# Kernel tuning notes

Measured on AMD Instinct MI355X. Metric: run time of the kernel, lower is better.

Reference implementation:

```python
import jax, jax.numpy as jnp
import numpy as np

B, R, C1, C2, C3, K, NC = 512, 200, 32, 32, 512, 8, 2
RATIO = 0.5
K1 = int(np.ceil(RATIO * R))    # 100 nodes kept after pool1
K2 = int(np.ceil(RATIO * K1))   # 50 nodes kept after pool2
EDGE_P = 0.1
NEG = -1e9
BN_EPS = 1e-5
LEAK = 0.01


def setup_inputs() -> dict:
    key = jax.random.key(0)
    ks = jax.random.split(key, 12)

    def lin_w(k, o, i):
        return (jax.random.normal(k, (o, i)) / np.sqrt(i)).astype(jnp.float32)

    return {
        "x": jax.random.normal(ks[0], (B, R, R), dtype=jnp.float32),
        "adj": jax.random.uniform(ks[1], (B, R, R), dtype=jnp.float32),
        "roi": jnp.arange(R, dtype=jnp.int32),
        # conv1 ROI-conditioned weight net: Linear(R->K) -> ReLU -> Linear(K->R*C1)
        "W1a": lin_w(ks[2], K, R), "b1a": jnp.zeros((K,), jnp.float32),
        "W2a": lin_w(ks[3], R * C1, K), "b2a": jnp.zeros((R * C1,), jnp.float32),
        "bias1": jnp.zeros((C1,), jnp.float32),
        # conv2 ROI-conditioned weight net: Linear(R->K) -> ReLU -> Linear(K->C1*C2)
        "W1b": lin_w(ks[4], K, R), "b1b": jnp.zeros((K,), jnp.float32),
        "W2b": lin_w(ks[5], C1 * C2, K), "b2b": jnp.zeros((C1 * C2,), jnp.float32),
        "bias2": jnp.zeros((C2,), jnp.float32),
        # TopK pooling projection vectors
        "wp1": jax.random.normal(ks[6], (C1,), dtype=jnp.float32),
        "wp2": jax.random.normal(ks[7], (C2,), dtype=jnp.float32),
        # MLP head
        "Wm1": lin_w(ks[8], C2, (C1 + C2) * 2), "bm1": jnp.zeros((C2,), jnp.float32),
        "g1": jnp.ones((C2,), jnp.float32), "be1": jnp.zeros((C2,), jnp.float32),
        "Wm2": lin_w(ks[9], C3, C2), "bm2": jnp.zeros((C3,), jnp.float32),
        "g2": jnp.ones((C3,), jnp.float32), "be2": jnp.zeros((C3,), jnp.float32),
        "Ws": lin_w(ks[10], NC, C3), "bs": jnp.zeros((NC,), jnp.float32),
    }


def _nn_table(W1, b1, W2, b2, cin, cout):
    # nn applied to one-hot ROI vectors == table lookup; build the full [R, cin, cout] table once.
    t = jax.nn.relu(W1.T + b1) @ W2.T + b2  # [R, cin*cout]
    return t.reshape(R, cin, cout)


def _gconv(x, w_adj, mask, w_node, bias):
    # per-node ROI-conditioned transform, then edge-softmax weighted aggregation
    if w_node.ndim == 3:   # shared table indexed by arange -> [R,cin,cout]
        xt = jnp.einsum('bni,nio->bno', x, w_node)
    else:                   # gathered per graph -> [B,n,cin,cout]
        xt = jnp.einsum('bni,bnio->bno', x, w_node)
    n = x.shape[1]
    eye = jnp.eye(n, dtype=bool)
    # remove self loops, add self loop with weight 1, softmax over incoming edges
    logits = jnp.where(mask & ~eye, w_adj, NEG)
    logits = jnp.where(eye, 1.0, logits)
    att = jax.nn.softmax(logits, axis=-1)  # row i = incoming edges of node i
    return jnp.einsum('bij,bjo->bio', att, xt) + bias


def _topk_pool(h, w_adj, mask, roi, w, k):
    s = jax.nn.sigmoid(h @ w / jnp.linalg.norm(w))  # [B, n]
    vals, perm = jax.lax.top_k(s, k)
    xs = jnp.take_along_axis(h, perm[:, :, None], axis=1) * vals[:, :, None]
    b = jnp.arange(h.shape[0])[:, None, None]
    w_sub = w_adj[b, perm[:, :, None], perm[:, None, :]]
    m_sub = mask[b, perm[:, :, None], perm[:, None, :]]
    roi_sub = roi[perm] if roi.ndim == 1 else jnp.take_along_axis(roi, perm, axis=1)
    return xs, w_sub, m_sub, roi_sub, vals


def _augment(w_adj, mask):
    # add_self_loops(fill=1) -> spspmm(A, A) -> remove_self_loops, in dense-batched form
    n = w_adj.shape[1]
    eye = jnp.eye(n, dtype=bool)
    wd = jnp.where(mask & ~eye, w_adj, 0.0)
    wd = jnp.where(eye, 1.0, wd)
    a2 = jnp.einsum('bij,bjk->bik', wd, wd)
    m2 = (a2 != 0.0) & ~eye
    a2 = jnp.where(eye, 0.0, a2)
    return a2, m2


def _mlp_block(y, Wl, bl, g, be):
    y = y @ Wl.T + bl
    y = jnp.where(y > 0, y, LEAK * y)          # LeakyReLU(0.01)
    mu = jnp.mean(y, axis=0)
    var = jnp.var(y, axis=0)                    # training-mode BatchNorm1d
    return g * (y - mu) * jax.lax.rsqrt(var + BN_EPS) + be


def _forward(x, adj, roi, W1a, b1a, W2a, b2a, bias1, W1b, b1b, W2b, b2b, bias2,
             wp1, wp2, Wm1, bm1, g1, be1, Wm2, bm2, g2, be2, Ws, bs):
    mask0 = adj < EDGE_P
    wtab1 = _nn_table(W1a, b1a, W2a, b2a, R, C1)   # [R, R, C1]
    h1 = _gconv(x, adj, mask0, wtab1[roi], bias1)  # [B, R, C1]
    x1, w1, m1, roi1, vals1 = _topk_pool(h1, adj, mask0, roi, wp1, K1)
    a_aug, m_aug = _augment(w1, m1)                 # 2-hop augmented adjacency
    wtab2 = _nn_table(W1b, b1b, W2b, b2b, C1, C2)  # [R, C1, C2]
    h2 = _gconv(x1, a_aug, m_aug, wtab2[roi1], bias2)  # [B, K1, C2]
    x2, _, _, _, vals2 = _topk_pool(h2, a_aug, m_aug, roi1, wp2, K2)
    # readout: [gmp, gap] per level, concatenated -> (C1+C2)*2 = 128
    feat = jnp.concatenate([x1.max(1), x1.mean(1), x2.max(1), x2.mean(1)], axis=-1)
    y = _mlp_block(feat, Wm1, bm1, g1, be1)
    y = _mlp_block(y, Wm2, bm2, g2, be2)
    logp = jax.nn.log_softmax(y @ Ws.T + bs, axis=-1)
    return logp, jax.nn.sigmoid(vals1), jax.nn.sigmoid(vals2)


def reference(x, adj, roi, W1a, b1a, W2a, b2a, bias1, W1b, b1b, W2b, b2b, bias2,
              wp1, wp2, Wm1, bm1, g1, be1, Wm2, bm2, g2, be2, Ws, bs):
    logp, s1, s2 = _forward(x, adj, roi, W1a, b1a, W2a, b2a, bias1,
                            W1b, b1b, W2b, b2b, bias2, wp1, wp2,
                            Wm1, bm1, g1, be1, Wm2, bm2, g2, be2, Ws, bs)
    return (logp, wp1, wp2, s1, s2)
```

## Files before the change

kernel.cpp:

```cpp
#include <hip/hip_runtime.h>
#include <math.h>

#define NB 512
#define RR 200
#define KK1 100
#define KK2 50

__device__ __forceinline__ float sigm(float v) { return 1.0f / (1.0f + expf(-v)); }

__global__ void k_tab(const float* __restrict__ W1, const float* __restrict__ b1,
                      const float* __restrict__ W2, const float* __restrict__ b2,
                      float* __restrict__ tab, int OUT) {
  int n = blockIdx.x;
  __shared__ float h[8];
  if (threadIdx.x < 8) {
    float v = W1[threadIdx.x * RR + n] + b1[threadIdx.x];
    h[threadIdx.x] = v > 0.f ? v : 0.f;
  }
  __syncthreads();
  for (int j = threadIdx.x; j < OUT; j += 256) {
    float acc = b2[j];
#pragma unroll
    for (int k = 0; k < 8; k++) acc += h[k] * W2[j * 8 + k];
    tab[(size_t)n * OUT + j] = acc;
  }
}

__global__ void k_norm(const float* __restrict__ wp1, const float* __restrict__ wp2,
                       float* __restrict__ norms) {
  int t = threadIdx.x;
  float a = (t < 32) ? wp1[t] * wp1[t] : 0.f;
  float b = (t < 32) ? wp2[t] * wp2[t] : 0.f;
  for (int s = 32; s; s >>= 1) { a += __shfl_xor(a, s); b += __shfl_xor(b, s); }
  if (t == 0) { norms[0] = sqrtf(a); norms[1] = sqrtf(b); }
}

__global__ __launch_bounds__(1024) void k_xt1(const float* __restrict__ x,
                                              const float* __restrict__ wtab1,
                                              float* __restrict__ xt1) {
  int n = blockIdx.x, t = threadIdx.x;
  __shared__ float wsm[6400];
  for (int idx = t; idx < 1600; idx += 1024)
    *(float4*)&wsm[idx * 4] = *(const float4*)(wtab1 + (size_t)n * 6400 + idx * 4);
  __syncthreads();
  int bg = t >> 3, og = t & 7;
  int b0 = bg * 4;
  const float* xp = x + (size_t)b0 * 40000 + (size_t)n * 200;
  float acc[4][4] = {};
  float4 A[4], Bf[4], N0[4] = {}, N1[4] = {};
#pragma unroll
  for (int r = 0; r < 4; r++) A[r] = *(const float4*)(xp + (size_t)r * 40000);
#pragma unroll
  for (int r = 0; r < 4; r++) Bf[r] = *(const float4*)(xp + (size_t)r * 40000 + 4);
  for (int g = 0; g < 50; g += 2) {
    int i = g * 4;
    if (g + 2 < 50) {
#pragma unroll
      for (int r = 0; r < 4; r++) N0[r] = *(const float4*)(xp + (size_t)r * 40000 + i + 8);
#pragma unroll
      for (int r = 0; r < 4; r++) N1[r] = *(const float4*)(xp + (size_t)r * 40000 + i + 12);
    }
#pragma unroll
    for (int k = 0; k < 4; k++) {
      float4 w4 = *(const float4*)&wsm[(i + k) * 32 + og * 4];
#pragma unroll
      for (int r = 0; r < 4; r++) {
        float xs = (&A[r].x)[k];
        acc[r][0] += xs * w4.x; acc[r][1] += xs * w4.y;
        acc[r][2] += xs * w4.z; acc[r][3] += xs * w4.w;
      }
    }
#pragma unroll
    for (int k = 0; k < 4; k++) {
      float4 w4 = *(const float4*)&wsm[(i + 4 + k) * 32 + og * 4];
#pragma unroll
      for (int r = 0; r < 4; r++) {
        float xs = (&Bf[r].x)[k];
        acc[r][0] += xs * w4.x; acc[r][1] += xs * w4.y;
        acc[r][2] += xs * w4.z; acc[r][3] += xs * w4.w;
      }
    }
#pragma unroll
    for (int r = 0; r < 4; r++) { A[r] = N0[r]; Bf[r] = N1[r]; }
  }
#pragma unroll
  for (int r = 0; r < 4; r++)
    *(float4*)(xt1 + (size_t)(b0 + r) * 6400 + (size_t)n * 32 + og * 4) =
        make_float4(acc[r][0], acc[r][1], acc[r][2], acc[r][3]);
}

__global__ __launch_bounds__(1024) void k_att1(const float* __restrict__ adj,
                                               const float* __restrict__ xt1,
                                               const float* __restrict__ bias1,
                                               const float* __restrict__ wp1,
                                               const float* __restrict__ norms,
                                               float* __restrict__ h1, float* __restrict__ sc1) {
  int t = threadIdx.x;
  __shared__ float2 pvj[16][4][49];
  __shared__ int cntS[16][4];
  int w = t >> 6, lane = t & 63;
  int rq = lane >> 4, cg = lane & 15;
  float2 biasv = *(const float2*)(bias1 + cg * 2);
  float2 wpv = *(const float2*)(wp1 + cg * 2);
  float nrm = norms[0];
  unsigned long long ltmask = (1ull << lane) - 1ull;
  int b = blockIdx.x;
  float av[4][4];
  {
    const float* abase = adj + (size_t)b * 40000 + (size_t)(w * 4) * 200;
#pragma unroll
    for (int r = 0; r < 4; r++)
#pragma unroll
      for (int s2 = 0; s2 < 4; s2++) {
        int j = lane + 64 * s2;
        av[r][s2] = (j < RR) ? __builtin_nontemporal_load(abase + r * 200 + j) : 1.0f;
      }
  }
  for (int rg = w; rg < 50; rg += 16) {
#pragma unroll
    for (int r = 0; r < 4; r++) {
      int i = rg * 4 + r;
      float e[4];
      bool nz[4];
#pragma unroll
      for (int s2 = 0; s2 < 4; s2++) {
        int j = lane + 64 * s2;
        float a = av[r][s2];
        bool keep = (j < RR) && ((j == i) || (a < 0.1f));
        float lg = (j == i) ? 1.0f : a;
        e[s2] = keep ? __expf(lg - 1.0f) : 0.f;
        nz[s2] = keep;
      }
      int base = 0;
#pragma unroll
      for (int s2 = 0; s2 < 4; s2++) {
        unsigned long long m = __ballot(nz[s2]);
        if (nz[s2]) pvj[w][r][base + __popcll(m & ltmask)] = make_float2(e[s2], (float)(lane + 64 * s2));
        base += __popcll(m);
      }
      if (lane == 0) cntS[w][r] = base;
    }
    int rg2 = rg + 16;
    if (rg2 < 50) {
      const float* abase = adj + (size_t)b * 40000 + (size_t)(rg2 * 4) * 200;
#pragma unroll
      for (int r = 0; r < 4; r++)
#pragma unroll
        for (int s2 = 0; s2 < 4; s2++) {
          int j = lane + 64 * s2;
          if (j < RR) av[r][s2] = __builtin_nontemporal_load(abase + r * 200 + j);
        }
    }
    int cnt = cntS[w][rq];
    const float* xtb = xt1 + (size_t)b * 6400 + cg * 2;
    float ax = 0.f, ay = 0.f, lsum = 0.f;
    for (int q = 0; q < cnt; q++) {
      float2 pe = pvj[w][rq][q];
      int jj = (int)pe.y;
      float2 xv = *(const float2*)(xtb + jj * 32);
      lsum += pe.x;
      ax += pe.x * xv.x;
      ay += pe.x * xv.y;
    }
    float inv = 1.0f / lsum;
    int i = rg * 4 + rq;
    float2 hv = make_float2(ax * inv + biasv.x, ay * inv + biasv.y);
    *(float2*)(h1 + ((size_t)b * RR + i) * 32 + cg * 2) = hv;
    float tt = hv.x * wpv.x + hv.y * wpv.y;
    tt += __shfl_xor(tt, 1); tt += __shfl_xor(tt, 2);
    tt += __shfl_xor(tt, 4); tt += __shfl_xor(tt, 8);
    if (cg == 0) sc1[b * RR + i] = sigm(tt / nrm);
  }
}

__global__ void k_top1(const float* __restrict__ sc1, int* __restrict__ perm1,
                       float* __restrict__ vals1, float* __restrict__ out_s1) {
  int b = blockIdx.x, t = threadIdx.x;
  __shared__ float s[RR];
  for (int i = t; i < RR; i += 256) s[i] = sc1[b * RR + i];
  __syncthreads();
  for (int i = t; i < RR; i += 256) {
    float si = s[i];
    int rank = 0;
    for (int j = 0; j < RR; j++) {
      float sj = s[j];
      rank += (sj > si) || (sj == si && j < i);
    }
    if (rank < KK1) {
      perm1[b * KK1 + rank] = i;
      vals1[b * KK1 + rank] = si;
      out_s1[b * KK1 + rank] = sigm(si);
    }
  }
}

__global__ __launch_bounds__(256) void k_stage2a(const float* __restrict__ h1,
                                                 const float* __restrict__ wtab2,
                                                 const int* __restrict__ perm1,
                                                 const float* __restrict__ vals1,
                                                 float* __restrict__ xt2,
                                                 float* __restrict__ feat) {
  int b = blockIdx.x, t = threadIdx.x;
  int kbase = blockIdx.y * 50;
  __shared__ float x1s[KK1 * 33];
  __shared__ int pk[KK1];
  __shared__ float vk[KK1];
  if (t < KK1) { pk[t] = perm1[b * KK1 + t]; vk[t] = vals1[b * KK1 + t]; }
  __syncthreads();
  for (int i = t; i < KK1 * 32; i += 256) {
    int k = i >> 5, o = i & 31;
    x1s[k * 33 + o] = h1[((size_t)b * RR + pk[k]) * 32 + o] * vk[k];
  }
  __syncthreads();
  if (blockIdx.y == 0 && t < 32) {
    float mx = -3e38f, sm = 0.f;
    for (int k = 0; k < KK1; k++) { float v = x1s[k * 33 + t]; mx = fmaxf(mx, v); sm += v; }
    feat[b * 128 + t] = mx;
    feat[b * 128 + 32 + t] = sm / 100.0f;
  }
  int w = t >> 6, lane = t & 63;
  int og = lane & 7, kq = lane >> 3;
#pragma unroll
  for (int pass = 0; pass < 2; pass++) {
    int kl = pass * 32 + w * 8 + kq;
    if (kl < 50) {
      int kg = kbase + kl;
      const float* W = wtab2 + (size_t)pk[kg] * 1024 + og * 4;
      float4 a4 = make_float4(0.f, 0.f, 0.f, 0.f);
#pragma unroll 8
      for (int ii = 0; ii < 32; ii++) {
        float4 w4 = *(const float4*)(W + ii * 32);
        float xs = x1s[kg * 33 + ii];
        a4.x += xs * w4.x; a4.y += xs * w4.y; a4.z += xs * w4.z; a4.w += xs * w4.w;
      }
      *(float4*)(xt2 + (size_t)b * 3200 + kg * 32 + og * 4) = a4;
    }
  }
}

__global__ __launch_bounds__(256) void k_wd(const float* __restrict__ adj,
                                            const int* __restrict__ perm1,
                                            float* __restrict__ wd) {
  int b = blockIdx.x, t = threadIdx.x;
  int g0 = blockIdx.y * 20;
  __shared__ float rowbuf[20][200];
  __shared__ int pk[KK1];
  if (t < KK1) pk[t] = perm1[b * KK1 + t];
  __syncthreads();
  for (int idx = t; idx < 4000; idx += 256) {
    int r = idx / 200, j = idx - r * 200;
    rowbuf[r][j] = adj[(size_t)b * 40000 + (size_t)pk[g0 + r] * 200 + j];
  }
  __syncthreads();
  for (int idx = t; idx < 2000; idx += 256) {
    int r = idx / 100, k2 = idx - r * 100;
    int k1 = g0 + r;
    float v;
    if (k1 == k2) v = 1.0f;
    else {
      float av = rowbuf[r][pk[k2]];
      v = (av < 0.1f) ? av : 0.0f;
    }
    wd[(size_t)b * (KK1 * KK1) + k1 * KK1 + k2] = v;
  }
}

__global__ __launch_bounds__(512) void k_stage2b(const float* __restrict__ wd,
                                                 const float* __restrict__ xt2,
                                                 const float* __restrict__ bias2,
                                                 const float* __restrict__ wp2,
                                                 const float* __restrict__ norms,
                                                 float* __restrict__ h2, float* __restrict__ sc2,
                                                 float* __restrict__ out_s2,
                                                 float* __restrict__ feat) {
  int b = blockIdx.x, t = threadIdx.x;
  __shared__ float wds[KK1][100];
  __shared__ float xts[KK1 * 32];
  __shared__ float pT[8][KK1][4];
  __shared__ int   nzidx[KK1][36];
  int w = t >> 6, lane = t & 63;
  unsigned long long ltmask = (1ull << lane) - 1ull;
  float bias_o = bias2[lane & 31];
  float wp_o = wp2[lane & 31];
  float nrm = norms[1];
  int k2a = lane;
  int k2b = lane + 64;
  bool vb = k2b < KK1;
  for (int i = t; i < KK1 * KK1; i += 512) ((float*)wds)[i] = wd[(size_t)b * (KK1 * KK1) + i];
  for (int idx = t; idx < 800; idx += 512)
    *(float4*)&xts[idx * 4] = *(const float4*)(xt2 + (size_t)b * 3200 + idx * 4);
  __syncthreads();
  for (int r = w; r < KK1; r += 8) {
    bool nz0 = (wds[r][lane] != 0.f);
    bool nz1 = (lane < KK1 - 64) && (wds[r][64 + lane] != 0.f);
    unsigned long long m0 = __ballot(nz0);
    unsigned long long m1 = __ballot(nz1);
    int c0 = __popcll(m0);
    int cnt = c0 + __popcll(m1);
    if (nz0) nzidx[r][__popcll(m0 & ltmask)] = lane;
    if (nz1) nzidx[r][c0 + __popcll(m1 & ltmask)] = 64 + lane;
    int pad = (4 - (cnt & 3)) & 3;
    if (lane < pad) nzidx[r][cnt + lane] = 0;
    if (lane == 0) nzidx[r][35] = cnt;
  }
  __syncthreads();
  for (int g = w; g < 25; g += 8) {
    int r0 = g * 4;
    float acc[4][2];
#pragma unroll
    for (int r = 0; r < 4; r++) {
      int k1 = r0 + r;
      int cnt = nzidx[k1][35];
      float s0 = 0.f, s1 = 0.f;
      for (int it = 0; it < cnt; it += 4) {
        int4 m4 = *(const int4*)&nzidx[k1][it];
        float a0 = wds[k1][m4.x];
        float a1 = (it + 1 < cnt) ? wds[k1][m4.y] : 0.f;
        float a2v = (it + 2 < cnt) ? wds[k1][m4.z] : 0.f;
        float a3 = (it + 3 < cnt) ? wds[k1][m4.w] : 0.f;
        s0 += a0 * wds[m4.x][k2a]; s1 += a0 * wds[m4.x][k2b];
        s0 += a1 * wds[m4.y][k2a]; s1 += a1 * wds[m4.y][k2b];
        s0 += a2v * wds[m4.z][k2a]; s1 += a2v * wds[m4.z][k2b];
        s0 += a3 * wds[m4.w][k2a]; s1 += a3 * wds[m4.w][k2b];
      }
      acc[r][0] = s0; acc[r][1] = s1;
    }
    float p0[4], p1[4], rs[4];
#pragma unroll
    for (int r = 0; r < 4; r++) {
      int k1 = r0 + r;
      float lv0 = (k1 == k2a) ? 1.0f : ((acc[r][0] != 0.0f) ? acc[r][0] : -1e9f);
      float lv1 = (k1 == k2b) ? 1.0f : ((acc[r][1] != 0.0f) ? acc[r][1] : -1e9f);
      float mx = vb ? fmaxf(lv0, lv1) : lv0;
      for (int s = 32; s; s >>= 1) mx = fmaxf(mx, __shfl_xor(mx, s));
      float e0 = expf(lv0 - mx);
      float e1 = vb ? expf(lv1 - mx) : 0.f;
      float ls = e0 + e1;
      for (int s = 32; s; s >>= 1) ls += __shfl_xor(ls, s);
      p0[r] = e0; p1[r] = e1; rs[r] = 1.0f / ls;
    }
    *(float4*)&pT[w][k2a][0] = make_float4(p0[0] * rs[0], p0[1] * rs[1], p0[2] * rs[2], p0[3] * rs[3]);
    if (vb) *(float4*)&pT[w][k2b][0] = make_float4(p1[0] * rs[0], p1[1] * rs[1], p1[2] * rs[2], p1[3] * rs[3]);
    int half = lane >> 5, o = lane & 31;
    float hv[4] = {0.f, 0.f, 0.f, 0.f};
    for (int jj = 0; jj < 50; jj++) {
      int j = half * 50 + jj;
      float4 pv = *(const float4*)&pT[w][j][0];
      float xv = xts[j * 32 + o];
      hv[0] += pv.x * xv; hv[1] += pv.y * xv; hv[2] += pv.z * xv; hv[3] += pv.w * xv;
    }
#pragma unroll
    for (int r = 0; r < 4; r++) hv[r] += __shfl_down(hv[r], 32);
    if (lane < 32) {
#pragma unroll
      for (int r = 0; r < 4; r++) {
        float h = hv[r] + bias_o;
        h2[((size_t)b * KK1 + (r0 + r)) * 32 + o] = h;
        float tt = h * wp_o;
        for (int s = 16; s; s >>= 1) tt += __shfl_xor(tt, s);
        if (lane == 0) sc2[b * KK1 + (r0 + r)] = sigm(tt / nrm);
      }
    }
  }
  __syncthreads();
  float* s = (float*)&pT[0][0][0];
  int* p2 = (int*)(s + 128);
  float* v2 = (float*)(p2 + 64);
  if (t < KK1) s[t] = sc2[b * KK1 + t];
  __syncthreads();
  if (t < KK1) {
    float si = s[t];
    int rank = 0;
    for (int j = 0; j < KK1; j++) {
      float sj = s[j];
      rank += (sj > si) || (sj == si && j < t);
    }
    if (rank < KK2) {
      p2[rank] = t;
      v2[rank] = si;
      out_s2[b * KK2 + rank] = sigm(si);
    }
  }
  __syncthreads();
  if (t < 32) {
    float mx = -3e38f, sm = 0.f;
    for (int k = 0; k < KK2; k++) {
      float v = h2[((size_t)b * KK1 + p2[k]) * 32 + t] * v2[k];
      mx = fmaxf(mx, v);
      sm += v;
    }
    feat[b * 128 + 64 + t] = mx;
    feat[b * 128 + 96 + t] = sm / 50.0f;
  }
}

__global__ void k_mlp1(const float* __restrict__ feat, const float* __restrict__ Wm1,
                       const float* __restrict__ bm1, float* __restrict__ y1) {
  __shared__ float Wt[128 * 32];
  __shared__ float f[8][128];
  int t = threadIdx.x;
  for (int i = t; i < 4096; i += 256) { int c = i >> 7, d = i & 127; Wt[d * 32 + c] = Wm1[i]; }
  int b0 = blockIdx.x * 8;
  for (int i = t; i < 1024; i += 256) f[i >> 7][i & 127] = feat[b0 * 128 + i];
  __syncthreads();
  int bl = t >> 5, c = t & 31;
  float acc = bm1[c];
#pragma unroll 4
  for (int d = 0; d < 128; d++) acc += f[bl][d] * Wt[d * 32 + c];
  y1[(b0 + bl) * 32 + c] = acc > 0.f ? acc : 0.01f * acc;
}

__global__ void k_bn(const float* __restrict__ y, int C, float* __restrict__ stats) {
  int c = blockIdx.x, t = threadIdx.x;
  __shared__ float ys[512];
  __shared__ float red[8];
  ys[t] = y[(size_t)t * C + c];
  ys[t + 256] = y[(size_t)(t + 256) * C + c];
  __syncthreads();
  float s = ys[t] + ys[t + 256];
  for (int d = 32; d; d >>= 1) s += __shfl_xor(s, d);
  if ((t & 63) == 0) red[t >> 6] = s;
  __syncthreads();
  float mu = (red[0] + red[1] + red[2] + red[3]) * (1.0f / 512.0f);
  float d0 = ys[t] - mu, d1 = ys[t + 256] - mu;
  float v = d0 * d0 + d1 * d1;
  for (int d = 32; d; d >>= 1) v += __shfl_xor(v, d);
  if ((t & 63) == 0) red[4 + (t >> 6)] = v;
  __syncthreads();
  if (t == 0) {
    float var = (red[4] + red[5] + red[6] + red[7]) * (1.0f / 512.0f);
    stats[c] = mu;
    stats[C + c] = rsqrtf(var + 1e-5f);
  }
}

__global__ void k_mlp2(const float* __restrict__ y1, const float* __restrict__ st1,
                       const float* __restrict__ g1, const float* __restrict__ be1,
                       const float* __restrict__ Wm2, const float* __restrict__ bm2,
                       float* __restrict__ y2) {
  __shared__ float yn[32];
  int b = blockIdx.x, t = threadIdx.x;
  if (t < 32) {
    float v = y1[b * 32 + t];
    yn[t] = g1[t] * (v - st1[t]) * st1[32 + t] + be1[t];
  }
  __syncthreads();
  for (int c = t; c < 512; c += 256) {
    float acc = bm2[c];
#pragma unroll
    for (int k = 0; k < 32; k++) acc += yn[k] * Wm2[c * 32 + k];
    y2[(size_t)b * 512 + c] = acc > 0.f ? acc : 0.01f * acc;
  }
}

__global__ void k_final(const float* __restrict__ y2, const float* __restrict__ st2,
                        const float* __restrict__ g2, const float* __restrict__ be2,
                        const float* __restrict__ Ws, const float* __restrict__ bs,
                        float* __restrict__ out) {
  int w = threadIdx.x >> 6, lane = threadIdx.x & 63;
  int b = blockIdx.x * 4 + w;
  float z0 = 0.f, z1 = 0.f;
  for (int c = lane; c < 512; c += 64) {
    float v = g2[c] * (y2[(size_t)b * 512 + c] - st2[c]) * st2[512 + c] + be2[c];
    z0 += v * Ws[c];
    z1 += v * Ws[512 + c];
  }
  for (int s = 32; s; s >>= 1) { z0 += __shfl_xor(z0, s); z1 += __shfl_xor(z1, s); }
  if (lane == 0) {
    z0 += bs[0];
    z1 += bs[1];
    float m = fmaxf(z0, z1);
    float lse = m + logf(expf(z0 - m) + expf(z1 - m));
    out[b * 2] = z0 - lse;
    out[b * 2 + 1] = z1 - lse;
  }
}

__global__ void k_copy(const float* __restrict__ wp1, const float* __restrict__ wp2,
                       float* __restrict__ out) {
  int t = threadIdx.x;
  if (t < 32) out[1024 + t] = wp1[t];
  else if (t < 64) out[1056 + (t - 32)] = wp2[t - 32];
}

extern "C" void kernel_launch(void* const* d_in, const int* in_sizes, int n_in,
                              void* d_out, int out_size, void* d_ws, size_t ws_size,
                              hipStream_t stream) {
  const float* x    = (const float*)d_in[0];
  const float* adj  = (const float*)d_in[1];
  const float* W1a  = (const float*)d_in[3];
  const float* b1a  = (const float*)d_in[4];
  const float* W2a  = (const float*)d_in[5];
  const float* b2a  = (const float*)d_in[6];
  const float* bias1= (const float*)d_in[7];
  const float* W1b  = (const float*)d_in[8];
  const float* b1b  = (const float*)d_in[9];
  const float* W2b  = (const float*)d_in[10];
  const float* b2b  = (const float*)d_in[11];
  const float* bias2= (const float*)d_in[12];
  const float* wp1  = (const float*)d_in[13];
  const float* wp2  = (const float*)d_in[14];
  const float* Wm1  = (const float*)d_in[15];
  const float* bm1  = (const float*)d_in[16];
  const float* g1   = (const float*)d_in[17];
  const float* be1  = (const float*)d_in[18];
  const float* Wm2  = (const float*)d_in[19];
  const float* bm2  = (const float*)d_in[20];
  const float* g2   = (const float*)d_in[21];
  const float* be2  = (const float*)d_in[22];
  const float* Ws   = (const float*)d_in[23];
  const float* bs   = (const float*)d_in[24];
  float* out = (float*)d_out;

  float* ws = (float*)d_ws;
  float* WTAB1 = ws;
  float* WTAB2 = WTAB1 + 1280000;
  float* NORMS = WTAB2 + 204800;
  float* XT1   = NORMS + 16;
  float* H1    = XT1 + 3276800;
  float* SC1   = H1 + 3276800;
  float* VALS1 = SC1 + 102400;
  int*   PERM1 = (int*)(VALS1 + 51200);
  float* XT2   = (float*)(PERM1 + 51200);
  float* WD    = XT2 + 1638400;
  float* H2    = WD + 5120000;
  float* SC2   = H2 + 1638400;
  float* FEAT  = SC2 + 51200;
  float* Y1    = FEAT + 65536;
  float* ST1   = Y1 + 16384;
  float* Y2    = ST1 + 64;
  float* ST2   = Y2 + 262144;

  k_tab<<<200, 256, 0, stream>>>(W1a, b1a, W2a, b2a, WTAB1, 6400);
  k_tab<<<200, 256, 0, stream>>>(W1b, b1b, W2b, b2b, WTAB2, 1024);
  k_norm<<<1, 64, 0, stream>>>(wp1, wp2, NORMS);
  k_xt1<<<200, 1024, 0, stream>>>(x, WTAB1, XT1);
  k_att1<<<512, 1024, 0, stream>>>(adj, XT1, bias1, wp1, NORMS, H1, SC1);
  k_top1<<<512, 256, 0, stream>>>(SC1, PERM1, VALS1, out + 1088);
  k_stage2a<<<dim3(512, 2), 256, 0, stream>>>(H1, WTAB2, PERM1, VALS1, XT2, FEAT);
  k_wd<<<dim3(512, 5), 256, 0, stream>>>(adj, PERM1, WD);
  k_stage2b<<<512, 512, 0, stream>>>(WD, XT2, bias2, wp2, NORMS, H2, SC2,
                                     out + 52288, FEAT);
  k_mlp1<<<64, 256, 0, stream>>>(FEAT, Wm1, bm1, Y1);
  k_bn<<<32, 256, 0, stream>>>(Y1, 32, ST1);
  k_mlp2<<<512, 256, 0, stream>>>(Y1, ST1, g1, be1, Wm2, bm2, Y2);
  k_bn<<<512, 256, 0, stream>>>(Y2, 512, ST2);
  k_final<<<128, 256, 0, stream>>>(Y2, ST2, g2, be2, Ws, bs, out);
  k_copy<<<1, 64, 0, stream>>>(wp1, wp2, out);
}
```

Measured before the change: 202.4 us.

## Split k_xt1 across batch tiles and stage x rows in shared memory

Changes k_xt1 from 200 blocks of 1024 threads, which read x directly from global with strided per-thread float4 loads, to a 200x8 grid of 128-thread blocks. Each block cooperatively loads a 64-batch by 200-element slice of x into padded shared memory before the matmul. The goal is coalesced global loads and more, smaller blocks for better distribution across CUs. In exchange, the 25.6KB weight table is reloaded 8 times per node and each block uses about 77KB of shared memory, which may limit occupancy.

Result: slower. 241.6 us (+19.4%).

```diff
diff --git a/kernel.cpp b/kernel.cpp
--- a/kernel.cpp
+++ b/kernel.cpp
@@ -35,58 +35,44 @@
   if (t == 0) { norms[0] = sqrtf(a); norms[1] = sqrtf(b); }
 }
 
-__global__ __launch_bounds__(1024) void k_xt1(const float* __restrict__ x,
-                                              const float* __restrict__ wtab1,
-                                              float* __restrict__ xt1) {
+__global__ __launch_bounds__(128) void k_xt1(const float* __restrict__ x,
+                                             const float* __restrict__ wtab1,
+                                             float* __restrict__ xt1) {
   int n = blockIdx.x, t = threadIdx.x;
   __shared__ float wsm[6400];
-  for (int idx = t; idx < 1600; idx += 1024)
+  __shared__ float xs[64][204];
+  int b0g = blockIdx.y * 64;
+  for (int idx = t; idx < 1600; idx += 128)
     *(float4*)&wsm[idx * 4] = *(const float4*)(wtab1 + (size_t)n * 6400 + idx * 4);
+  for (int idx = t; idx < 3200; idx += 128) {
+    int b = idx / 50, q = idx - b * 50;
+    *(float4*)&xs[b][q * 4] =
+        *(const float4*)(x + (size_t)(b0g + b) * 40000 + (size_t)n * 200 + q * 4);
+  }
   __syncthreads();
   int bg = t >> 3, og = t & 7;
-  int b0 = bg * 4;
-  const float* xp = x + (size_t)b0 * 40000 + (size_t)n * 200;
   float acc[4][4] = {};
-  float4 A[4], Bf[4], N0[4] = {}, N1[4] = {};
-#pragma unroll
-  for (int r = 0; r < 4; r++) A[r] = *(const float4*)(xp + (size_t)r * 40000);
-#pragma unroll
-  for (int r = 0; r < 4; r++) Bf[r] = *(const float4*)(xp + (size_t)r * 40000 + 4);
-  for (int g = 0; g < 50; g += 2) {
-    int i = g * 4;
-    if (g + 2 < 50) {
-#pragma unroll
-      for (int r = 0; r < 4; r++) N0[r] = *(const float4*)(xp + (size_t)r * 40000 + i + 8);
-#pragma unroll
-      for (int r = 0; r < 4; r++) N1[r] = *(const float4*)(xp + (size_t)r * 40000 + i + 12);
-    }
+  for (int i = 0; i < 200; i += 4) {
+    float4 xv[4];
+#pragma unroll
+    for (int r = 0; r < 4; r++) xv[r] = *(const float4*)&xs[bg + 16 * r][i];
 #pragma unroll
     for (int k = 0; k < 4; k++) {
       float4 w4 = *(const float4*)&wsm[(i + k) * 32 + og * 4];
 #pragma unroll
       for (int r = 0; r < 4; r++) {
-        float xs = (&A[r].x)[k];
-        acc[r][0] += xs * w4.x; acc[r][1] += xs * w4.y;
-        acc[r][2] += xs * w4.z; acc[r][3] += xs * w4.w;
-      }
-    }
-#pragma unroll
-    for (int k = 0; k < 4; k++) {
-      float4 w4 = *(const float4*)&wsm[(i + 4 + k) * 32 + og * 4];
-#pragma unroll
-      for (int r = 0; r < 4; r++) {
-        float xs = (&Bf[r].x)[k];
-        acc[r][0] += xs * w4.x; acc[r][1] += xs * w4.y;
-        acc[r][2] += xs * w4.z; acc[r][3] += xs * w4.w;
-      }
-    }
-#pragma unroll
-    for (int r = 0; r < 4; r++) { A[r] = N0[r]; Bf[r] = N1[r]; }
-  }
-#pragma unroll
-  for (int r = 0; r < 4; r++)
-    *(float4*)(xt1 + (size_t)(b0 + r) * 6400 + (size_t)n * 32 + og * 4) =
+        float s = (&xv[r].x)[k];
+        acc[r][0] += s * w4.x; acc[r][1] += s * w4.y;
+        acc[r][2] += s * w4.z; acc[r][3] += s * w4.w;
+      }
+    }
+  }
+#pragma unroll
+  for (int r = 0; r < 4; r++) {
+    int b = b0g + bg + 16 * r;
+    *(float4*)(xt1 + (size_t)b * 6400 + (size_t)n * 32 + og * 4) =
         make_float4(acc[r][0], acc[r][1], acc[r][2], acc[r][3]);
+  }
 }
 
 __global__ __launch_bounds__(1024) void k_att1(const float* __restrict__ adj,
@@ -534,7 +520,7 @@
   k_tab<<<200, 256, 0, stream>>>(W1a, b1a, W2a, b2a, WTAB1, 6400);
   k_tab<<<200, 256, 0, stream>>>(W1b, b1b, W2b, b2b, WTAB2, 1024);
   k_norm<<<1, 64, 0, stream>>>(wp1, wp2, NORMS);
-  k_xt1<<<200, 1024, 0, stream>>>(x, WTAB1, XT1);
+  k_xt1<<<dim3(200, 8), 128, 0, stream>>>(x, WTAB1, XT1);
   k_att1<<<512, 1024, 0, stream>>>(adj, XT1, bias1, wp1, NORMS, H1, SC1);
   k_top1<<<512, 256, 0, stream>>>(SC1, PERM1, VALS1, out + 1088);
   k_stage2a<<<dim3(512, 2), 256, 0, stream>>>(H1, WTAB2, PERM1, VALS1, XT2, FEAT);
```
